# Performance work log

Hardware: AMD Instinct MI355X
Metric: run time of the kernel (lower is better)

Reference implementation:

```python
import jax, jax.numpy as jnp
import numpy as np

B, LQ, LKV = 4, 512, 4096
IN_DIM, N_HEADS, DIM_HEAD = 1024, 16, 64
INNER = N_HEADS * DIM_HEAD


def setup_inputs() -> dict:
    key = jax.random.key(0)
    ks = jax.random.split(key, 6)
    q = jax.random.normal(ks[0], (B, LQ, IN_DIM), dtype=jnp.float32)
    kv = jax.random.normal(ks[1], (B, LKV, IN_DIM), dtype=jnp.float32)
    mask = jax.random.randint(ks[2], (B, 1, 1, LKV), 0, 2).astype(jnp.bool_)
    w_scale = 0.02
    Wq = jax.random.normal(ks[3], (IN_DIM, INNER), dtype=jnp.float32) * w_scale
    Wkv = jax.random.normal(ks[4], (IN_DIM, 2 * INNER), dtype=jnp.float32) * w_scale
    Wo = jax.random.normal(ks[5], (INNER, IN_DIM), dtype=jnp.float32) * w_scale
    return {"q": q, "kv": kv, "mask": mask, "Wq": Wq, "Wkv": Wkv, "Wo": Wo}


def reference(q, kv, mask, Wq, Wkv, Wo):
    # projections
    qp = q @ Wq                                  # [B, LQ, INNER]
    kvp = kv @ Wkv                               # [B, LKV, 2*INNER]
    # split heads
    qh = qp.reshape(B, LQ, N_HEADS, DIM_HEAD).transpose(0, 2, 1, 3)   # [B,H,LQ,D]
    kvh = kvp.reshape(B, LKV, N_HEADS, 2 * DIM_HEAD).transpose(0, 2, 1, 3)
    kh, vh = kvh[..., :DIM_HEAD], kvh[..., DIM_HEAD:]                 # [B,H,LKV,D]
    scale = jnp.sqrt(jnp.asarray(DIM_HEAD, dtype=qh.dtype))
    scores = jnp.einsum("bhqd,bhkd->bhqk", qh, kh) / scale            # [B,H,LQ,LKV]
    scores = jnp.where(mask, -jnp.inf, scores)
    weights = jax.nn.softmax(scores, axis=-1)
    context = jnp.einsum("bhqk,bhkd->bhqd", weights, vh)              # [B,H,LQ,D]
    context = context.transpose(0, 2, 1, 3).reshape(B, LQ, INNER)
    return context @ Wo                                               # [B,LQ,IN_DIM]
```

## Files before the change

kernel.cpp:

```cpp
#include <hip/hip_runtime.h>
#include <hip/hip_bf16.h>
#include <math.h>

#define B_      4
#define LQ_     512
#define LKV_    4096
#define IN_DIM_ 1024
#define NH_     16
#define DH_     64
#define INNER_  1024

typedef _Float16 f16x8 __attribute__((ext_vector_type(8)));
typedef _Float16 f16x4 __attribute__((ext_vector_type(4)));
typedef float    f32x4 __attribute__((ext_vector_type(4)));

#define GLDS(gp, lp) __builtin_amdgcn_global_load_lds( \
    (const __attribute__((address_space(1))) void*)(gp), \
    (__attribute__((address_space(3))) void*)(lp), 16, 0, 0)

__global__ __launch_bounds__(256) void scan_mask(const int* __restrict__ mask,
                                                 int* __restrict__ pidx,
                                                 int* __restrict__ cnt) {
  __shared__ int wsum_s[4];
  int b = blockIdx.x, tid = threadIdx.x;
  const int* mb = mask + b * LKV_;
  int base = tid * 16;
  int vals[16];
#pragma unroll
  for (int i = 0; i < 4; ++i) {
    int4 v = *(const int4*)(mb + base + i * 4);
    vals[i * 4 + 0] = v.x; vals[i * 4 + 1] = v.y;
    vals[i * 4 + 2] = v.z; vals[i * 4 + 3] = v.w;
  }
  int s = 0;
#pragma unroll
  for (int j = 0; j < 16; ++j) s += (vals[j] == 0);
  int lane = tid & 63, wave = tid >> 6;
  int inc = s;
#pragma unroll
  for (int d = 1; d < 64; d <<= 1) {
    int v = __shfl_up(inc, d);
    if (lane >= d) inc += v;
  }
  if (lane == 63) wsum_s[wave] = inc;
  __syncthreads();
  int woff = 0;
#pragma unroll
  for (int w = 0; w < 4; ++w)
    if (w < wave) woff += wsum_s[w];
  if (tid == 255) cnt[b] = woff + inc;
  int run = woff + inc - s;
#pragma unroll
  for (int i = 0; i < 4; ++i) {
    int4 o;
    int* op = &o.x;
#pragma unroll
    for (int j = 0; j < 4; ++j) { op[j] = run; run += (vals[i * 4 + j] == 0); }
    *(int4*)(pidx + b * LKV_ + base + i * 4) = o;
  }
}

__device__ __forceinline__ void transpose_tile(const float* __restrict__ in,
                                               _Float16* __restrict__ out,
                                               int K, int N, int xb, int yb,
                                               float (*t)[33]) {
  int bn = xb * 32, bk = yb * 32;
  int tx = threadIdx.x & 31, ty = threadIdx.x >> 5;
#pragma unroll
  for (int i = 0; i < 4; ++i) {
    int r = ty + i * 8;
    t[r][tx] = in[(size_t)(bk + r) * N + bn + tx];
  }
  __syncthreads();
#pragma unroll
  for (int i = 0; i < 4; ++i) {
    int r = ty + i * 8;
    out[(size_t)(bn + r) * K + bk + tx] = (_Float16)t[tx][r];
  }
}

__global__ __launch_bounds__(256) void prep_compact(
    const float* __restrict__ kv, const float* __restrict__ q,
    const float* __restrict__ Wq, const float* __restrict__ Wkv,
    const float* __restrict__ Wo, const int* __restrict__ mask,
    const int* __restrict__ pidx,
    _Float16* __restrict__ kv16, _Float16* __restrict__ q16,
    _Float16* __restrict__ Wqt, _Float16* __restrict__ Wkvt,
    _Float16* __restrict__ Wot) {
  __shared__ float t[32][33];
  const int tid = threadIdx.x;
  for (int id = blockIdx.x; id < 22528; id += (int)gridDim.x) {
    if (id < 16384) {
      if (mask[id] == 0) {
        int b = id >> 12;
        int dst = b * LKV_ + pidx[id];
        float4 v = ((const float4*)(kv + (size_t)id * IN_DIM_))[tid];
        f16x4 h = {(_Float16)v.x, (_Float16)v.y, (_Float16)v.z, (_Float16)v.w};
        ((f16x4*)(kv16 + (size_t)dst * IN_DIM_))[tid] = h;
      }
    } else if (id < 18432) {
      int i = (id - 16384) * 256 + tid;
      float4 v = ((const float4*)q)[i];
      f16x4 h = {(_Float16)v.x, (_Float16)v.y, (_Float16)v.z, (_Float16)v.w};
      ((f16x4*)q16)[i] = h;
    } else if (id < 19456) {
      int l = id - 18432;
      transpose_tile(Wq, Wqt, 1024, 1024, l & 31, l >> 5, t);
    } else if (id < 21504) {
      int l = id - 19456;
      transpose_tile(Wkv, Wkvt, 1024, 2048, l & 63, l >> 6, t);
    } else {
      int l = id - 21504;
      transpose_tile(Wo, Wot, 1024, 1024, l & 31, l >> 5, t);
    }
    __syncthreads();
  }
}

__global__ __launch_bounds__(256, 4) void proj_f16(
    const _Float16* __restrict__ kv16, const _Float16* __restrict__ Wkvt,
    const _Float16* __restrict__ q16, const _Float16* __restrict__ Wqt,
    _Float16* __restrict__ qp16, _Float16* __restrict__ Kp,
    _Float16* __restrict__ Vt, const int* __restrict__ Cnt) {
  const int id = blockIdx.x;
  const bool is_kv = (id < 2048);
  int brow, bcol;
  const _Float16 *Ab, *Bb;
  if (is_kv) {
    bcol = (id & 15) * 128;
    brow = (id >> 4) * 128;
    if ((brow & 4095) >= Cnt[brow >> 12]) return;
    Ab = kv16 + (size_t)brow * 1024;
    Bb = Wkvt + (size_t)bcol * 1024;
  } else {
    int l = id - 2048;
    bcol = (l & 7) * 128;
    brow = (l >> 3) * 128;
    Ab = q16 + (size_t)brow * 1024;
    Bb = Wqt + (size_t)bcol * 1024;
  }
  __shared__ _Float16 As[128 * 64];
  __shared__ _Float16 Bs[128 * 64];
  const int tid = threadIdx.x;
  const int wave = tid >> 6, lane = tid & 63;
  const int quad = lane >> 4, l16 = lane & 15;
  const int wm = (wave & 1) * 64, wn = (wave >> 1) * 64;
  const int ro8 = lane >> 3, c8 = lane & 7;

  f32x4 acc[4][4];
#pragma unroll
  for (int i = 0; i < 4; ++i)
#pragma unroll
    for (int j = 0; j < 4; ++j) acc[i][j] = (f32x4){0.f, 0.f, 0.f, 0.f};

  for (int k0 = 0; k0 < 1024; k0 += 64) {
    __syncthreads();
#pragma unroll
    for (int i = 0; i < 4; ++i) {
      int rbase = wave * 32 + i * 8;
      int row = rbase + ro8;
      int g = c8 ^ (row & 7);
      GLDS(Ab + (size_t)row * 1024 + k0 + g * 8, &As[rbase * 64]);
      GLDS(Bb + (size_t)row * 1024 + k0 + g * 8, &Bs[rbase * 64]);
    }
    __syncthreads();
#pragma unroll
    for (int ks = 0; ks < 2; ++ks) {
      f16x8 af[4], bf[4];
      int c = ks * 4 + quad;
#pragma unroll
      for (int mt = 0; mt < 4; ++mt) {
        int r = wm + mt * 16 + l16;
        af[mt] = *(const f16x8*)&As[r * 64 + ((c ^ (r & 7)) * 8)];
        int rb = wn + mt * 16 + l16;
        bf[mt] = *(const f16x8*)&Bs[rb * 64 + ((c ^ (rb & 7)) * 8)];
      }
#pragma unroll
      for (int mt = 0; mt < 4; ++mt)
#pragma unroll
        for (int nt = 0; nt < 4; ++nt)
          acc[mt][nt] = __builtin_amdgcn_mfma_f32_16x16x32_f16(af[mt], bf[nt], acc[mt][nt], 0, 0, 0);
    }
  }

#pragma unroll
  for (int mt = 0; mt < 4; ++mt) {
    int row0 = brow + wm + mt * 16 + quad * 4;
#pragma unroll
    for (int nt = 0; nt < 4; ++nt) {
      int col = bcol + wn + nt * 16 + l16;
      f32x4 v = acc[mt][nt];
      if (is_kv) {
        int h = col >> 7, w64 = col & 63;
        if ((col & 127) < 64) {
#pragma unroll
          for (int r = 0; r < 4; ++r)
            Kp[(size_t)(row0 + r) * INNER_ + h * 64 + w64] = (_Float16)v[r];
        } else {
          int b = row0 >> 12, key = row0 & 4095;
          f16x4 pk = {(_Float16)v[0], (_Float16)v[1], (_Float16)v[2], (_Float16)v[3]};
          *(f16x4*)&Vt[((size_t)((b * NH_ + h) * DH_) + w64) * LKV_ + key] = pk;
        }
      } else {
#pragma unroll
        for (int r = 0; r < 4; ++r)
          qp16[(size_t)(row0 + r) * 1024 + col] = (_Float16)v[r];
      }
    }
  }
}

__global__ __launch_bounds__(256, 2) void attn_f16(
    const _Float16* __restrict__ qp, const _Float16* __restrict__ Kp,
    const _Float16* __restrict__ Vt, const int* __restrict__ cnt,
    _Float16* __restrict__ ctx) {
  const int idx = blockIdx.x;
  const int bh = idx & 63, qt = idx >> 6;
  const int b = bh >> 4, h = bh & 15;
  __shared__ _Float16 Ks[128 * 64];
  __shared__ _Float16 Vts[64 * 128];
  __shared__ _Float16 Pl[64][136];

  const int tid = threadIdx.x;
  const int wave = tid >> 6, lane = tid & 63;
  const int quad = lane >> 4, l16 = lane & 15;
  const int ro8 = lane >> 3, gch8 = (lane & 7) ^ (ro8 & 7);
  const int ro16 = lane >> 4, ch16 = lane & 15;

  const int qrow = b * LQ_ + qt * 64 + wave * 16 + l16;
  const _Float16* qpr = qp + (size_t)qrow * INNER_ + h * DH_;
  f16x8 qf[2];
  qf[0] = *(const f16x8*)(qpr + quad * 8);
  qf[1] = *(const f16x8*)(qpr + 32 + quad * 8);

  const int c_act = cnt[b];
  const int tiles = (c_act + 127) >> 7;

  float l_run = 0.f;
  f32x4 oacc[4];
#pragma unroll
  for (int i = 0; i < 4; ++i) oacc[i] = (f32x4){0.f, 0.f, 0.f, 0.f};

  const _Float16* kb = Kp + (size_t)(b * LKV_) * INNER_ + h * DH_;
  const _Float16* vb = Vt + (size_t)((b * NH_ + h) * DH_) * LKV_;

  for (int t = 0; t < tiles; ++t) {
    __syncthreads();
#pragma unroll
    for (int i = 0; i < 4; ++i) {
      int rbase = wave * 32 + i * 8;
      GLDS(kb + (size_t)(t * 128 + rbase + ro8) * INNER_ + gch8 * 8, &Ks[rbase * 64]);
    }
#pragma unroll
    for (int i = 0; i < 4; ++i) {
      int rbase = wave * 16 + i * 4;
      int row = rbase + ro16;
      int gch = ch16 ^ (row & 15);
      GLDS(vb + (size_t)row * LKV_ + t * 128 + gch * 8, &Vts[rbase * 128]);
    }
    __syncthreads();

    f32x4 sacc[8];
#pragma unroll
    for (int i = 0; i < 8; ++i) sacc[i] = (f32x4){0.f, 0.f, 0.f, 0.f};
#pragma unroll
    for (int ks = 0; ks < 2; ++ks) {
      int c = ks * 4 + quad;
#pragma unroll
      for (int mt = 0; mt < 8; ++mt) {
        int krow = mt * 16 + l16;
        f16x8 af = *(const f16x8*)&Ks[krow * 64 + ((c ^ (krow & 7)) * 8)];
        sacc[mt] = __builtin_amdgcn_mfma_f32_16x16x32_f16(af, qf[ks], sacc[mt], 0, 0, 0);
      }
    }
    const int lim = c_act - t * 128;
    float psloc = 0.f;
#pragma unroll
    for (int mt = 0; mt < 8; ++mt) {
      f16x4 pk;
#pragma unroll
      for (int r = 0; r < 4; ++r) {
        int key = mt * 16 + quad * 4 + r;
        float s = sacc[mt][r] * 0.125f;
        if (key >= lim) s = -1e30f;
        float p = __expf(s - 8.0f);
        psloc += p;
        pk[r] = (_Float16)p;
      }
      *(f16x4*)&Pl[wave * 16 + l16][mt * 16 + quad * 4] = pk;
    }
    psloc += __shfl_xor(psloc, 16);
    psloc += __shfl_xor(psloc, 32);
    l_run += psloc;
#pragma unroll
    for (int ks = 0; ks < 4; ++ks) {
      int c = ks * 4 + quad;
      f16x8 bf = *(const f16x8*)&Pl[wave * 16 + l16][ks * 32 + quad * 8];
#pragma unroll
      for (int mt = 0; mt < 4; ++mt) {
        int drow = mt * 16 + l16;
        f16x8 af = *(const f16x8*)&Vts[drow * 128 + ((c ^ (drow & 15)) * 8)];
        oacc[mt] = __builtin_amdgcn_mfma_f32_16x16x32_f16(af, bf, oacc[mt], 0, 0, 0);
      }
    }
  }

  const float inv = (l_run > 0.f) ? 1.f / l_run : 0.f;
  _Float16* cb = ctx + (size_t)qrow * INNER_ + h * DH_;
#pragma unroll
  for (int mt = 0; mt < 4; ++mt) {
    f16x4 o;
#pragma unroll
    for (int r = 0; r < 4; ++r) o[r] = (_Float16)(oacc[mt][r] * inv);
    *(f16x4*)(cb + mt * 16 + quad * 4) = o;
  }
}

__global__ __launch_bounds__(256, 2) void gemm_out(
    const _Float16* __restrict__ A, const _Float16* __restrict__ Bt,
    float* __restrict__ C) {
  const int brow = blockIdx.y * 64, bcol = blockIdx.x * 64;
  __shared__ _Float16 As[64 * 64];
  __shared__ _Float16 Bs[64 * 64];
  const int tid = threadIdx.x;
  const int wave = tid >> 6, lane = tid & 63;
  const int quad = lane >> 4, l16 = lane & 15;
  const int wm = (wave & 1) * 32, wn = (wave >> 1) * 32;
  const int ro8 = lane >> 3, c8 = lane & 7;

  f32x4 acc[2][2];
#pragma unroll
  for (int i = 0; i < 2; ++i)
#pragma unroll
    for (int j = 0; j < 2; ++j) acc[i][j] = (f32x4){0.f, 0.f, 0.f, 0.f};

  const _Float16* Ab = A + (size_t)brow * 1024;
  const _Float16* Bb = Bt + (size_t)bcol * 1024;

  for (int k0 = 0; k0 < 1024; k0 += 64) {
    __syncthreads();
#pragma unroll
    for (int i = 0; i < 2; ++i) {
      int rbase = wave * 16 + i * 8;
      int row = rbase + ro8;
      int g = c8 ^ (row & 7);
      GLDS(Ab + (size_t)row * 1024 + k0 + g * 8, &As[rbase * 64]);
      GLDS(Bb + (size_t)row * 1024 + k0 + g * 8, &Bs[rbase * 64]);
    }
    __syncthreads();
#pragma unroll
    for (int ks = 0; ks < 2; ++ks) {
      f16x8 af[2], bf[2];
      int c = ks * 4 + quad;
#pragma unroll
      for (int mt = 0; mt < 2; ++mt) {
        int r = wm + mt * 16 + l16;
        af[mt] = *(const f16x8*)&As[r * 64 + ((c ^ (r & 7)) * 8)];
        int rb = wn + mt * 16 + l16;
        bf[mt] = *(const f16x8*)&Bs[rb * 64 + ((c ^ (rb & 7)) * 8)];
      }
#pragma unroll
      for (int mt = 0; mt < 2; ++mt)
#pragma unroll
        for (int nt = 0; nt < 2; ++nt)
          acc[mt][nt] = __builtin_amdgcn_mfma_f32_16x16x32_f16(af[mt], bf[nt], acc[mt][nt], 0, 0, 0);
    }
  }

#pragma unroll
  for (int mt = 0; mt < 2; ++mt) {
    int row0 = brow + wm + mt * 16 + quad * 4;
#pragma unroll
    for (int nt = 0; nt < 2; ++nt) {
      int col = bcol + wn + nt * 16 + l16;
      f32x4 v = acc[mt][nt];
#pragma unroll
      for (int r = 0; r < 4; ++r) C[(size_t)(row0 + r) * 1024 + col] = v[r];
    }
  }
}

extern "C" void kernel_launch(void* const* d_in, const int* in_sizes, int n_in,
                              void* d_out, int out_size, void* d_ws, size_t ws_size,
                              hipStream_t stream) {
  const float* q   = (const float*)d_in[0];
  const float* kv  = (const float*)d_in[1];
  const int* mask  = (const int*)d_in[2];
  const float* Wq  = (const float*)d_in[3];
  const float* Wkv = (const float*)d_in[4];
  const float* Wo  = (const float*)d_in[5];
  float* out = (float*)d_out;

  _Float16* p = (_Float16*)d_ws;
  _Float16* q16   = p; p += (size_t)2048 * 1024;
  _Float16* kv16  = p; p += (size_t)16384 * 1024;
  _Float16* Wqt   = p; p += (size_t)1024 * 1024;
  _Float16* Wkvt  = p; p += (size_t)2048 * 1024;
  _Float16* Wot   = p; p += (size_t)1024 * 1024;
  _Float16* qp16  = p; p += (size_t)2048 * 1024;
  _Float16* Kp    = p; p += (size_t)16384 * 1024;
  _Float16* Vt    = p; p += (size_t)16384 * 1024;
  _Float16* ctx16 = p; p += (size_t)2048 * 1024;
  int* pidx = (int*)p;
  int* cnt  = pidx + 16384;

  scan_mask<<<4, 256, 0, stream>>>(mask, pidx, cnt);
  prep_compact<<<2816, 256, 0, stream>>>(kv, q, Wq, Wkv, Wo, mask, pidx,
                                         kv16, q16, Wqt, Wkvt, Wot);
  proj_f16<<<2176, 256, 0, stream>>>(kv16, Wkvt, q16, Wqt, qp16, Kp, Vt, cnt);
  attn_f16<<<512, 256, 0, stream>>>(qp16, Kp, Vt, cnt, ctx16);
  gemm_out<<<dim3(16, 32), 256, 0, stream>>>(ctx16, Wot, out);
}
```

Measured before the change: 223.6 us.

## Double-buffer LDS tiles in projection GEMM with async global-to-LDS prefetch

Doubles the shared-memory A/B tiles in the projection GEMM so the next k-slice is issued via global_load_lds while the current slice is multiplied on MFMA, using vmcnt waits and raw barriers in place of syncthreads. The aim is to hide global load latency behind compute. In exchange LDS use doubles to 64KB per block and launch bounds drop from 4 to 2 blocks per CU, which lowers occupancy. The vmcnt(8) count relies on each stage issuing exactly 8 loads per thread.

```diff
diff --git a/kernel.cpp b/kernel.cpp
--- a/kernel.cpp
+++ b/kernel.cpp
@@ -117,7 +117,7 @@
   }
 }
 
-__global__ __launch_bounds__(256, 4) void proj_f16(
+__global__ __launch_bounds__(256, 2) void proj_f16(
     const _Float16* __restrict__ kv16, const _Float16* __restrict__ Wkvt,
     const _Float16* __restrict__ q16, const _Float16* __restrict__ Wqt,
     _Float16* __restrict__ qp16, _Float16* __restrict__ Kp,
@@ -139,8 +139,8 @@
     Ab = q16 + (size_t)brow * 1024;
     Bb = Wqt + (size_t)bcol * 1024;
   }
-  __shared__ _Float16 As[128 * 64];
-  __shared__ _Float16 Bs[128 * 64];
+  __shared__ _Float16 As[2][128 * 64];
+  __shared__ _Float16 Bs[2][128 * 64];
   const int tid = threadIdx.x;
   const int wave = tid >> 6, lane = tid & 63;
   const int quad = lane >> 4, l16 = lane & 15;
@@ -153,17 +153,17 @@
 #pragma unroll
     for (int j = 0; j < 4; ++j) acc[i][j] = (f32x4){0.f, 0.f, 0.f, 0.f};
 
-  for (int k0 = 0; k0 < 1024; k0 += 64) {
-    __syncthreads();
+  auto stage = [&](int p, int k0) {
 #pragma unroll
     for (int i = 0; i < 4; ++i) {
       int rbase = wave * 32 + i * 8;
       int row = rbase + ro8;
       int g = c8 ^ (row & 7);
-      GLDS(Ab + (size_t)row * 1024 + k0 + g * 8, &As[rbase * 64]);
-      GLDS(Bb + (size_t)row * 1024 + k0 + g * 8, &Bs[rbase * 64]);
-    }
-    __syncthreads();
+      GLDS(Ab + (size_t)row * 1024 + k0 + g * 8, &As[p][rbase * 64]);
+      GLDS(Bb + (size_t)row * 1024 + k0 + g * 8, &Bs[p][rbase * 64]);
+    }
+  };
+  auto compute = [&](int p) {
 #pragma unroll
     for (int ks = 0; ks < 2; ++ks) {
       f16x8 af[4], bf[4];
@@ -171,9 +171,9 @@
 #pragma unroll
       for (int mt = 0; mt < 4; ++mt) {
         int r = wm + mt * 16 + l16;
-        af[mt] = *(const f16x8*)&As[r * 64 + ((c ^ (r & 7)) * 8)];
+        af[mt] = *(const f16x8*)&As[p][r * 64 + ((c ^ (r & 7)) * 8)];
         int rb = wn + mt * 16 + l16;
-        bf[mt] = *(const f16x8*)&Bs[rb * 64 + ((c ^ (rb & 7)) * 8)];
+        bf[mt] = *(const f16x8*)&Bs[p][rb * 64 + ((c ^ (rb & 7)) * 8)];
       }
 #pragma unroll
       for (int mt = 0; mt < 4; ++mt)
@@ -181,6 +181,21 @@
         for (int nt = 0; nt < 4; ++nt)
           acc[mt][nt] = __builtin_amdgcn_mfma_f32_16x16x32_f16(af[mt], bf[nt], acc[mt][nt], 0, 0, 0);
     }
+  };
+
+  stage(0, 0);
+#pragma unroll
+  for (int t = 0; t < 16; ++t) {
+    const int cur = t & 1;
+    if (t < 15) {
+      stage(cur ^ 1, (t + 1) * 64);
+      asm volatile("s_waitcnt vmcnt(8)" ::: "memory");
+    } else {
+      asm volatile("s_waitcnt vmcnt(0)" ::: "memory");
+    }
+    __builtin_amdgcn_s_barrier();
+    compute(cur);
+    if (t < 15) __builtin_amdgcn_s_barrier();
   }
 
 #pragma unroll
```

After: 230.5 us. 3.1% more time.
